# Kernel optimization log

Measured on AMD Instinct MI355X. Metric: run time of the kernel, lower is better.

Reference implementation:

```python
import jax, jax.numpy as jnp
import numpy as np

B, T, C = 1, 4096, 1024   # batch, seq, n_embd
E, K = 64, 8              # num_experts, router top-k
G, TG = 8, 4              # n_group, topk_group
H, HS = 512, 2048         # expert hidden, shared-expert hidden
STD = 0.02


def setup_inputs() -> dict:
    key = jax.random.key(0)
    ks = jax.random.split(key, 9)
    return {
        "x": jax.random.normal(ks[0], (B, T, C), jnp.float32),
        "router_w": jax.random.normal(ks[1], (E, C), jnp.float32) * (C ** -0.5),
        "e_bias": jnp.zeros((E,), jnp.float32),  # e_score_correction_bias buffer
        "gate_w": jax.random.normal(ks[2], (E, C, H), jnp.float32) * STD,
        "up_w": jax.random.normal(ks[3], (E, C, H), jnp.float32) * STD,
        "down_w": jax.random.normal(ks[4], (E, H, C), jnp.float32) * STD,
        "sh_gate_w": jax.random.normal(ks[5], (C, HS), jnp.float32) * STD,
        "sh_up_w": jax.random.normal(ks[6], (C, HS), jnp.float32) * STD,
        "sh_down_w": jax.random.normal(ks[7], (HS, C), jnp.float32) * STD,
    }


def _route(xf, router_w, e_bias):
    # grouped sigmoid top-k routing with score-correction bias (group_limited_greedy)
    S = xf.shape[0]
    scores = jax.nn.sigmoid(xf @ router_w.T)          # [S,E], raw sigmoid scores
    sb = scores + e_bias                               # biased scores (selection only)
    epg = E // G
    # per-group score = sum of top (K // topk_group) biased scores in that group
    grp = jax.lax.top_k(sb.reshape(S, G, epg), K // TG)[0].sum(-1)   # [S,G]
    gidx = jax.lax.top_k(grp, TG)[1]                                 # [S,TG]
    gmask = jnp.zeros((S, G), bool).at[jnp.arange(S)[:, None], gidx].set(True)
    emask = jnp.repeat(gmask, epg, axis=1)                           # [S,E]
    masked = jnp.where(emask, sb, -jnp.inf)
    topk_idx = jax.lax.top_k(masked, K)[1]                           # [S,K]
    w = jnp.take_along_axis(scores, topk_idx, axis=1)                # raw scores gathered
    w = w / (w.sum(-1, keepdims=True) + 1e-20)                       # norm_topk_prob
    return topk_idx, w


def reference(x, router_w, e_bias, gate_w, up_w, down_w, sh_gate_w, sh_up_w, sh_down_w):
    Bq, Tq, Cq = x.shape
    xf = x.reshape(Bq * Tq, Cq)
    # always-on shared expert (SwiGLU)
    shared = (jax.nn.silu(xf @ sh_gate_w) * (xf @ sh_up_w)) @ sh_down_w
    topk_idx, w = _route(xf, router_w, e_bias)
    fe = topk_idx.reshape(-1)                          # [S*K] expert id per routed row
    order = jnp.argsort(fe, stable=True)               # sort rows by expert (grouped)
    tok = order // K                                   # source token of each sorted row
    sorted_x = xf[tok]                                 # [S*K, C]
    group_sizes = jnp.bincount(fe, length=E).astype(jnp.int32)
    # grouped GEMMs (== torch._grouped_mm / bmm-over-buckets in the original)
    g = jax.lax.ragged_dot(sorted_x, gate_w, group_sizes)
    u = jax.lax.ragged_dot(sorted_x, up_w, group_sizes)
    h = jax.nn.silu(g) * u
    o = jax.lax.ragged_dot(h, down_w, group_sizes)     # [S*K, C]
    o = o * w.reshape(-1)[order][:, None]              # weight by routing prob
    routed = jnp.zeros_like(xf).at[tok].add(o)         # combine back per token
    return (shared + routed).reshape(Bq, Tq, Cq)
```

## Files before the change

kernel.cpp:

```cpp
#include <hip/hip_runtime.h>
#include <hip/hip_bf16.h>
#include <stdint.h>


#define S_TOK 4096
#define C_DIM 1024
#define E_NUM 64
#define H_DIM 512
#define HS_DIM 2048
#define ROWS_TOTAL (S_TOK * 8)
#define T_TILES 320
#define NB_ROUTED_F (T_TILES * 8)
#define NB_SHARED_F (32 * 32)
#define NB_ROUTED_D (T_TILES * 8)
#define NB_SHARED_D (32 * 8)
#define NB_SCATTER  (ROWS_TOTAL / 256)

typedef __attribute__((ext_vector_type(8))) short short8;
typedef __attribute__((ext_vector_type(4))) float f32x4;
typedef __attribute__((ext_vector_type(2))) unsigned int uint2v;

static __device__ __forceinline__ unsigned short f2bf(float f) {
    union { float f; uint32_t u; } v; v.f = f;
    uint32_t u = v.u;
    u += 0x7fffu + ((u >> 16) & 1u);
    return (unsigned short)(u >> 16);
}

static __device__ __forceinline__ uint32_t cvtpk(float a, float b) {
    uint32_t r;
    asm("v_cvt_pk_bf16_f32 %0, %1, %2" : "=v"(r) : "v"(a), "v"(b));
    return r;
}

static __device__ __forceinline__ void gl2lds16(const void* g, void* l) {
    __builtin_amdgcn_global_load_lds(
        (const __attribute__((address_space(1))) uint32_t*)g,
        (__attribute__((address_space(3))) uint32_t*)l, 16, 0, 0);
}

static __device__ __forceinline__ uint2v tr64(unsigned addr) {
    uint2v r;
    asm volatile("ds_read_b64_tr_b16 %0, %1" : "=v"(r) : "v"(addr));
    return r;
}

__global__ __launch_bounds__(256)
void router_topk_k(const float* __restrict__ x, const float* __restrict__ rw,
                   const float* __restrict__ ebias,
                   int* __restrict__ topk_idx, float* __restrict__ topk_w,
                   int* __restrict__ counts, int* __restrict__ done,
                   int* __restrict__ base, int* __restrict__ cursor,
                   int* __restrict__ tile_e, int* __restrict__ tile_m0) {
    int t0 = blockIdx.x * 32;
    __shared__ float xs[32][36];
    __shared__ float wsm[64][36];
    __shared__ float scf[32][64];
    __shared__ int last_blk;
    int t = threadIdx.x;
    int tx = t & 15, ty = t >> 4;
    float acc[2][4] = {};
    for (int k0 = 0; k0 < C_DIM; k0 += 32) {
        {
            int r = t >> 3, c = t & 7;
            *(float4*)&xs[r][c * 4] = *(const float4*)(x + (size_t)(t0 + r) * C_DIM + k0 + c * 4);
        }
        #pragma unroll
        for (int i = 0; i < 2; i++) {
            int idx = t + 256 * i;
            int r = idx >> 3, c = idx & 7;
            *(float4*)&wsm[r][c * 4] = *(const float4*)(rw + (size_t)r * C_DIM + k0 + c * 4);
        }
        __syncthreads();
        #pragma unroll
        for (int kk = 0; kk < 32; kk += 4) {
            float4 a0 = *(const float4*)&xs[ty * 2 + 0][kk];
            float4 a1 = *(const float4*)&xs[ty * 2 + 1][kk];
            #pragma unroll
            for (int j = 0; j < 4; j++) {
                float4 b = *(const float4*)&wsm[tx * 4 + j][kk];
                acc[0][j] += a0.x * b.x + a0.y * b.y + a0.z * b.z + a0.w * b.w;
                acc[1][j] += a1.x * b.x + a1.y * b.y + a1.z * b.z + a1.w * b.w;
            }
        }
        __syncthreads();
    }
    #pragma unroll
    for (int i = 0; i < 2; i++)
        #pragma unroll
        for (int j = 0; j < 4; j++)
            scf[ty * 2 + i][tx * 4 + j] = 1.f / (1.f + __expf(-acc[i][j]));
    __syncthreads();

    int lane = t & 63, w = t >> 6;
    float eb = ebias[lane];
    for (int r = 0; r < 8; r++) {
        int lt = w * 8 + r;
        int tok = t0 + lt;
        float sc = scf[lt][lane];
        float sb = sc + eb;
        float m1 = sb, m2 = -1e30f;
        #pragma unroll
        for (int off = 1; off <= 4; off <<= 1) {
            float o1 = __shfl_xor(m1, off);
            float o2 = __shfl_xor(m2, off);
            float hi = fmaxf(m1, o1), lo = fminf(m1, o1);
            m2 = fmaxf(lo, fmaxf(m2, o2));
            m1 = hi;
        }
        float grp = m1 + m2;
        float grpv[8];
        #pragma unroll
        for (int g = 0; g < 8; g++) grpv[g] = __shfl(grp, g * 8);
        unsigned gsel = 0;
        #pragma unroll
        for (int k = 0; k < 4; k++) {
            float best = -1e30f; int bi = 0;
            #pragma unroll
            for (int g = 0; g < 8; g++)
                if (!((gsel >> g) & 1) && grpv[g] > best) { best = grpv[g]; bi = g; }
            gsel |= 1u << bi;
        }
        float val = ((gsel >> (lane >> 3)) & 1) ? sb : -1e30f;
        int idx[8]; float sv[8]; float wsum = 0.f;
        #pragma unroll
        for (int k = 0; k < 8; k++) {
            uint32_t u = __float_as_uint(val);
            uint32_t mu = (u & 0x80000000u) ? ~u : (u | 0x80000000u);
            unsigned long long key = ((unsigned long long)mu << 6) | (unsigned long long)(63 - lane);
            #pragma unroll
            for (int off = 32; off; off >>= 1) {
                unsigned long long ok = __shfl_xor(key, off);
                if (ok > key) key = ok;
            }
            int win = 63 - (int)(key & 63ull);
            idx[k] = win;
            sv[k] = __shfl(sc, win);
            wsum += sv[k];
            if (lane == win) val = -1e30f;
        }
        float inv = 1.f / (wsum + 1e-20f);
        if (lane < 8) {
            topk_idx[tok * 8 + lane] = idx[lane];
            topk_w[tok * 8 + lane] = sv[lane] * inv;
            atomicAdd(&counts[idx[lane]], 1);
        }
    }

    __threadfence();
    __syncthreads();
    if (t == 0) last_blk = (atomicAdd(done, 1) == (int)gridDim.x - 1) ? 1 : 0;
    __syncthreads();
    if (last_blk && t < 64) {
        __threadfence();
        int e = t;
        int c = atomicAdd(&counts[e], 0);
        int s = c;
        #pragma unroll
        for (int off = 1; off < 64; off <<= 1) {
            int o = __shfl_up(s, off);
            if (e >= off) s += o;
        }
        int ex = s - c;
        base[e] = ex;
        cursor[e] = ex;
        int nt = (c + 127) >> 7;
        int ts = nt;
        #pragma unroll
        for (int off = 1; off < 64; off <<= 1) {
            int o = __shfl_up(ts, off);
            if (e >= off) ts += o;
        }
        int tb = ts - nt;
        for (int i = 0; i < nt; i++) { tile_e[tb + i] = e; tile_m0[tb + i] = i * 128; }
        int total = __shfl(ts, 63);
        for (int j = total + e; j < T_TILES; j += 64) tile_e[j] = -1;
    }
}

__global__ __launch_bounds__(256)
void scatter_cvt_k(const int* __restrict__ topk_idx, const float* __restrict__ topk_w,
                   int* __restrict__ cursor, int* __restrict__ row_token,
                   float* __restrict__ row_wgt, int* __restrict__ pos_of,
                   const float* __restrict__ i0, unsigned short* __restrict__ o0, int n0,
                   const float* __restrict__ i1, unsigned short* __restrict__ o1, int n1,
                   const float* __restrict__ i2, unsigned short* __restrict__ o2, int n2,
                   const float* __restrict__ i3, unsigned short* __restrict__ o3, int n3,
                   const float* __restrict__ i4, unsigned short* __restrict__ o4, int n4,
                   const float* __restrict__ i5, unsigned short* __restrict__ o5, int n5,
                   const float* __restrict__ i6, unsigned short* __restrict__ o6, int n6) {
    int bid = blockIdx.x;
    if (bid < NB_SCATTER) {
        int i = bid * 256 + threadIdx.x;
        int e = topk_idx[i];
        int pos = atomicAdd(&cursor[e], 1);
        row_token[pos] = i >> 3;
        row_wgt[pos] = topk_w[i];
        pos_of[i] = pos;
        return;
    }
    int g = (bid - NB_SCATTER) * 256 + threadIdx.x;
    const float* in; unsigned short* out;
    if (g < n0) { in = i0; out = o0; }
    else { g -= n0;
    if (g < n1) { in = i1; out = o1; }
    else { g -= n1;
    if (g < n2) { in = i2; out = o2; }
    else { g -= n2;
    if (g < n3) { in = i3; out = o3; }
    else { g -= n3;
    if (g < n4) { in = i4; out = o4; }
    else { g -= n4;
    if (g < n5) { in = i5; out = o5; }
    else { g -= n5;
    if (g >= n6) return;
    in = i6; out = o6; } } } } } }
    float4 v0 = ((const float4*)in)[4 * g];
    float4 v1 = ((const float4*)in)[4 * g + 1];
    float4 v2 = ((const float4*)in)[4 * g + 2];
    float4 v3 = ((const float4*)in)[4 * g + 3];
    uint32_t pk[8];
    pk[0] = cvtpk(v0.x, v0.y); pk[1] = cvtpk(v0.z, v0.w);
    pk[2] = cvtpk(v1.x, v1.y); pk[3] = cvtpk(v1.z, v1.w);
    pk[4] = cvtpk(v2.x, v2.y); pk[5] = cvtpk(v2.z, v2.w);
    pk[6] = cvtpk(v3.x, v3.y); pk[7] = cvtpk(v3.z, v3.w);
    ((uint4*)out)[2 * g]     = *(uint4*)&pk[0];
    ((uint4*)out)[2 * g + 1] = *(uint4*)&pk[4];
}

__global__ __launch_bounds__(256)
void combine_k(const float* __restrict__ O, const int* __restrict__ pos_of,
               float* __restrict__ out) {
    int t = blockIdx.x;
    int c = threadIdx.x;
    float4 s = ((const float4*)(out + (size_t)t * C_DIM))[c];
    int p[8];
    #pragma unroll
    for (int k = 0; k < 8; k++) p[k] = pos_of[t * 8 + k];
    #pragma unroll
    for (int k = 0; k < 8; k++) {
        float4 v = ((const float4*)(O + (size_t)p[k] * C_DIM))[c];
        s.x += v.x; s.y += v.y; s.z += v.z; s.w += v.w;
    }
    ((float4*)(out + (size_t)t * C_DIM))[c] = s;
}

__global__ __launch_bounds__(256, 3)
void fused_all_k(const short* __restrict__ xb,
                 const short* __restrict__ gate_b, const short* __restrict__ up_b,
                 const short* __restrict__ shg_b, const short* __restrict__ shu_b,
                 unsigned short* __restrict__ Hr, unsigned short* __restrict__ Hs,
                 const int* __restrict__ counts, const int* __restrict__ base,
                 const int* __restrict__ row_token,
                 const int* __restrict__ tile_e, const int* __restrict__ tile_m0) {
    constexpr int K = C_DIM;
    constexpr int NC = 4;

    int bid = blockIdx.x;
    bool routed = bid < NB_ROUTED_F;
    const short* B1; const short* B2; unsigned short* Cout;
    int m0, n0, Mrows, rowbase, N;
    if (routed) {
        int ti = bid >> 3;
        int e = tile_e[ti];
        if (e < 0) return;
        m0 = tile_m0[ti]; n0 = (bid & 7) * 64;
        Mrows = counts[e]; rowbase = base[e];
        N = H_DIM;
        B1 = gate_b + (size_t)e * H_DIM * K;
        B2 = up_b   + (size_t)e * H_DIM * K;
        Cout = Hr;
    } else {
        int s = bid - NB_ROUTED_F;
        m0 = (s >> 5) * 128; n0 = (s & 31) * 64;
        Mrows = S_TOK; rowbase = 0;
        N = HS_DIM;
        B1 = shg_b; B2 = shu_b;
        Cout = Hs;
    }

    __shared__ short As[3 * 4096];
    __shared__ short Bs1[3 * 2048];
    __shared__ short Bs2[3 * 2048];

    int tid = threadIdx.x;
    int lane = tid & 63, w = tid >> 6;
    int wr = w >> 1, wc = w & 1;
    int quad = lane >> 4, l16 = lane & 15;
    int sr = lane >> 2, sc = lane & 3;

    const short* aptr[2];
    #pragma unroll
    for (int i = 0; i < 2; i++) {
        int row = w * 32 + i * 16 + sr;
        int mrow = m0 + row;
        int cl = mrow < Mrows ? mrow : (Mrows - 1);
        size_t arow = routed ? (size_t)row_token[rowbase + cl] : (size_t)cl;
        aptr[i] = xb + arow * K + sc * 8;
    }

    const short* b1ptr;
    const short* b2ptr;
    {
        int L = lane;
        int r = (L & 7) >> 1, c = (L & 1) * 8;
        int kc = w * 2 + (L >> 5);
        int nc = (L >> 3) & 3;
        b1ptr = B1 + (size_t)(kc * 4 + r) * N + n0 + nc * 16 + c;
        b2ptr = B2 + (size_t)(kc * 4 + r) * N + n0 + nc * 16 + c;
    }
    const size_t bstep = (size_t)32 * N;

    f32x4 acc1[4][2] = {};
    f32x4 acc2[4][2] = {};

    const int nk = K >> 5;
    auto stage = [&](int slot) {
        #pragma unroll
        for (int i = 0; i < 2; i++) {
            gl2lds16(aptr[i], &As[slot * 4096 + (w * 32 + i * 16) * 32]);
            aptr[i] += 32;
        }
        gl2lds16(b1ptr, &Bs1[slot * 2048 + w * 512]); b1ptr += bstep;
        gl2lds16(b2ptr, &Bs2[slot * 2048 + w * 512]); b2ptr += bstep;
    };
    stage(0);
    stage(1);

    unsigned trb1 = (unsigned)(size_t)&Bs1[0] + (unsigned)(quad * 2 * NC * 128 + l16 * 8);
    unsigned trb2 = (unsigned)(size_t)&Bs2[0] + (unsigned)(quad * 2 * NC * 128 + l16 * 8);
    auto rdB = [&](unsigned trb, int slot, int nb) -> short8 {
        unsigned a0 = trb + (unsigned)(slot * 4096 + nb * 128);
        uint2v lo = tr64(a0);
        uint2v hi = tr64(a0 + NC * 128);
        union { uint32_t u[4]; short8 s; } u;
        u.u[0] = lo[0]; u.u[1] = lo[1]; u.u[2] = hi[0]; u.u[3] = hi[1];
        return u.s;
    };

    int slot = 0, nslot = 2;
    for (int t = 0; t < nk; t++) {
        if (t + 1 < nk) {
            asm volatile("s_waitcnt vmcnt(4)" ::: "memory");
        } else {
            asm volatile("s_waitcnt vmcnt(0)" ::: "memory");
        }
        __builtin_amdgcn_s_barrier();
        __builtin_amdgcn_sched_barrier(0);

        if (t + 2 < nk) stage(nslot);

        short8 a[4], b1[2], b2[2];
        #pragma unroll
        for (int i = 0; i < 4; i++)
            a[i] = *(const short8*)&As[slot * 4096 + (wr * 64 + i * 16 + l16) * 32 + quad * 8];
        #pragma unroll
        for (int j = 0; j < 2; j++) {
            int nb = wc * 2 + j;
            b1[j] = rdB(trb1, slot, nb);
            b2[j] = rdB(trb2, slot, nb);
        }
        asm volatile("s_waitcnt lgkmcnt(0)" ::: "memory");
        __builtin_amdgcn_sched_barrier(0);
        #pragma unroll
        for (int i = 0; i < 4; i++)
            #pragma unroll
            for (int j = 0; j < 2; j++) {
                acc1[i][j] = __builtin_amdgcn_mfma_f32_16x16x32_bf16(a[i], b1[j], acc1[i][j], 0, 0, 0);
                acc2[i][j] = __builtin_amdgcn_mfma_f32_16x16x32_bf16(a[i], b2[j], acc2[i][j], 0, 0, 0);
            }
        slot = (slot == 2) ? 0 : slot + 1;
        nslot = (nslot == 2) ? 0 : nslot + 1;
    }

    #pragma unroll
    for (int i = 0; i < 4; i++) {
        #pragma unroll
        for (int rr = 0; rr < 4; rr++) {
            int row = m0 + wr * 64 + i * 16 + quad * 4 + rr;
            if (row >= Mrows) continue;
            size_t orow = (size_t)(rowbase + row);
            #pragma unroll
            for (int j = 0; j < 2; j++) {
                int n = n0 + wc * 32 + j * 16 + l16;
                float v = acc1[i][j][rr];
                float u = acc2[i][j][rr];
                float h = v / (1.f + __expf(-v)) * u;
                Cout[orow * N + n] = f2bf(h);
            }
        }
    }
}

__global__ __launch_bounds__(256, 3)
void down_all_k(const short* __restrict__ Hr, const short* __restrict__ Hs,
                const short* __restrict__ down_b, const short* __restrict__ shd_b,
                float* __restrict__ O, float* __restrict__ out,
                const int* __restrict__ counts, const int* __restrict__ base,
                const float* __restrict__ row_wgt,
                const int* __restrict__ tile_e, const int* __restrict__ tile_m0) {
    constexpr int N = C_DIM;
    constexpr int NC = 8;
    constexpr int BS = 128 * 32;

    int bid = blockIdx.x;
    bool shared_e = bid < NB_SHARED_D;
    const short* A; const short* B1; float* Cout;
    int m0, n0, Mrows, rowbase, K;
    if (shared_e) {
        m0 = (bid >> 3) * 128; n0 = (bid & 7) * 128;
        Mrows = S_TOK; rowbase = 0;
        K = HS_DIM;
        A = Hs;
        B1 = shd_b;
        Cout = out;
    } else {
        int rb = bid - NB_SHARED_D;
        int ti = rb >> 3;
        int e = tile_e[ti];
        if (e < 0) return;
        m0 = tile_m0[ti]; n0 = (rb & 7) * 128;
        Mrows = counts[e]; rowbase = base[e];
        K = H_DIM;
        A = Hr;
        B1 = down_b + (size_t)e * N * H_DIM;
        Cout = O;
    }

    __shared__ short As[3 * 4096];
    __shared__ short Bs1[3 * BS];

    int tid = threadIdx.x;
    int lane = tid & 63, w = tid >> 6;
    int wr = w >> 1, wc = w & 1;
    int quad = lane >> 4, l16 = lane & 15;
    int sr = lane >> 2, sc = lane & 3;

    const short* aptr[2];
    #pragma unroll
    for (int i = 0; i < 2; i++) {
        int row = w * 32 + i * 16 + sr;
        int mrow = m0 + row;
        int cl = mrow < Mrows ? mrow : (Mrows - 1);
        aptr[i] = A + (size_t)(rowbase + cl) * K + sc * 8;
    }

    const short* b1ptr[2];
    {
        int L = lane;
        int r = (L & 7) >> 1, c = (L & 1) * 8;
        int nc = L >> 3;
        #pragma unroll
        for (int i = 0; i < 2; i++) {
            int kc = w * 2 + i;
            b1ptr[i] = B1 + (size_t)(kc * 4 + r) * N + n0 + nc * 16 + c;
        }
    }
    const size_t bstep = (size_t)32 * N;

    f32x4 acc1[4][4] = {};

    const int nk = K >> 5;
    auto stage = [&](int slot) {
        #pragma unroll
        for (int i = 0; i < 2; i++) {
            gl2lds16(aptr[i], &As[slot * 4096 + (w * 32 + i * 16) * 32]);
            aptr[i] += 32;
        }
        #pragma unroll
        for (int i = 0; i < 2; i++) {
            gl2lds16(b1ptr[i], &Bs1[slot * BS + (w * 2 + i) * 512]);
            b1ptr[i] += bstep;
        }
    };
    stage(0);
    stage(1);

    unsigned trb1 = (unsigned)(size_t)&Bs1[0] + (unsigned)(quad * 2 * NC * 128 + l16 * 8);
    auto rdB = [&](int slot, int nb) -> short8 {
        unsigned a0 = trb1 + (unsigned)(slot * BS * 2 + nb * 128);
        uint2v lo = tr64(a0);
        uint2v hi = tr64(a0 + NC * 128);
        union { uint32_t u[4]; short8 s; } u;
        u.u[0] = lo[0]; u.u[1] = lo[1]; u.u[2] = hi[0]; u.u[3] = hi[1];
        return u.s;
    };

    int slot = 0, nslot = 2;
    for (int t = 0; t < nk; t++) {
        if (t + 1 < nk) {
            asm volatile("s_waitcnt vmcnt(4)" ::: "memory");
        } else {
            asm volatile("s_waitcnt vmcnt(0)" ::: "memory");
        }
        __builtin_amdgcn_s_barrier();
        __builtin_amdgcn_sched_barrier(0);

        if (t + 2 < nk) stage(nslot);

        short8 a[4], b1[4];
        #pragma unroll
        for (int i = 0; i < 4; i++)
            a[i] = *(const short8*)&As[slot * 4096 + (wr * 64 + i * 16 + l16) * 32 + quad * 8];
        #pragma unroll
        for (int j = 0; j < 4; j++)
            b1[j] = rdB(slot, wc * 4 + j);
        asm volatile("s_waitcnt lgkmcnt(0)" ::: "memory");
        __builtin_amdgcn_sched_barrier(0);
        #pragma unroll
        for (int i = 0; i < 4; i++)
            #pragma unroll
            for (int j = 0; j < 4; j++)
                acc1[i][j] = __builtin_amdgcn_mfma_f32_16x16x32_bf16(a[i], b1[j], acc1[i][j], 0, 0, 0);
        slot = (slot == 2) ? 0 : slot + 1;
        nslot = (nslot == 2) ? 0 : nslot + 1;
    }

    #pragma unroll
    for (int i = 0; i < 4; i++) {
        #pragma unroll
        for (int rr = 0; rr < 4; rr++) {
            int row = m0 + wr * 64 + i * 16 + quad * 4 + rr;
            if (row >= Mrows) continue;
            size_t orow = (size_t)(rowbase + row);
            float scl = shared_e ? 1.f : row_wgt[rowbase + row];
            #pragma unroll
            for (int j = 0; j < 4; j++) {
                int n = n0 + wc * 64 + j * 16 + l16;
                Cout[orow * N + n] = acc1[i][j][rr] * scl;
            }
        }
    }
}

extern "C" void kernel_launch(void* const* d_in, const int* in_sizes, int n_in,
                              void* d_out, int out_size, void* d_ws, size_t ws_size,
                              hipStream_t stream) {
    const float* x        = (const float*)d_in[0];
    const float* router_w = (const float*)d_in[1];
    const float* e_bias   = (const float*)d_in[2];
    const float* gate_w   = (const float*)d_in[3];
    const float* up_w     = (const float*)d_in[4];
    const float* down_w   = (const float*)d_in[5];
    const float* sh_gate  = (const float*)d_in[6];
    const float* sh_up    = (const float*)d_in[7];
    const float* sh_down  = (const float*)d_in[8];
    float* out = (float*)d_out;
    char* ws = (char*)d_ws;

    int*   counts    = (int*)(ws);
    int*   base      = (int*)(ws + 256);
    int*   cursor    = (int*)(ws + 512);
    int*   done      = (int*)(ws + 768);
    int*   topk_idx  = (int*)(ws + 1024);
    float* topk_w    = (float*)(ws + 1024 + 131072);
    int*   row_token = (int*)(ws + 1024 + 2 * 131072);
    float* row_wgt   = (float*)(ws + 1024 + 3 * 131072);
    int*   pos_of    = (int*)(ws + 1664 * 1024);
    int*   tile_e    = (int*)(ws + 1800 * 1024);
    int*   tile_m0   = (int*)(ws + 1808 * 1024);
    const size_t MB = 1u << 20;
    unsigned short* xb        = (unsigned short*)(ws + 2 * MB);
    unsigned short* Hs        = (unsigned short*)(ws + 10 * MB);
    unsigned short* Hr        = (unsigned short*)(ws + 26 * MB);
    unsigned short* sh_gate_b = (unsigned short*)(ws + 58 * MB);
    unsigned short* sh_up_b   = (unsigned short*)(ws + 62 * MB);
    unsigned short* sh_down_b = (unsigned short*)(ws + 66 * MB);
    unsigned short* gate_b    = (unsigned short*)(ws + 70 * MB);
    unsigned short* up_b      = (unsigned short*)(ws + 134 * MB);
    unsigned short* down_b    = (unsigned short*)(ws + 198 * MB);
    float* O = (float*)(ws + 70 * MB);

    hipMemsetAsync(ws, 0, 1024, stream);

    router_topk_k<<<S_TOK / 32, 256, 0, stream>>>(
        x, router_w, e_bias, topk_idx, topk_w, counts, done,
        base, cursor, tile_e, tile_m0);

    const int NX = S_TOK * C_DIM / 16;
    const int NW = E_NUM * C_DIM * H_DIM / 16;
    const int NS = C_DIM * HS_DIM / 16;
    const int NTOT = NX + 3 * NW + 3 * NS;
    scatter_cvt_k<<<NB_SCATTER + (NTOT + 255) / 256, 256, 0, stream>>>(
        topk_idx, topk_w, cursor, row_token, row_wgt, pos_of,
        x, xb, NX, gate_w, gate_b, NW, up_w, up_b, NW, down_w, down_b, NW,
        sh_gate, sh_gate_b, NS, sh_up, sh_up_b, NS, sh_down, sh_down_b, NS);

    fused_all_k<<<NB_ROUTED_F + NB_SHARED_F, 256, 0, stream>>>(
        (const short*)xb, (const short*)gate_b, (const short*)up_b,
        (const short*)sh_gate_b, (const short*)sh_up_b, Hr, Hs,
        counts, base, row_token, tile_e, tile_m0);

    down_all_k<<<NB_SHARED_D + NB_ROUTED_D, 256, 0, stream>>>(
        (const short*)Hr, (const short*)Hs, (const short*)down_b, (const short*)sh_down_b,
        O, out, counts, base, row_wgt, tile_e, tile_m0);

    combine_k<<<S_TOK, 256, 0, stream>>>(O, pos_of, out);
}
```

Baseline: 888.3 us.

## Convert fp32 weights to bf16 inside GEMM kernels instead of a separate pass

Removes the separate conversion of all expert and shared weights to bf16 and has the gate/up and down GEMM kernels load fp32 weights directly into registers, convert them, and write swizzled bf16 tiles to LDS. The B path becomes register-staged double buffering in place of global_load_lds plus transposed LDS reads. This removes a full read-and-write pass over roughly 200MB of weights, but the GEMMs now read fp32 weights (twice the bytes), and weights shared by several tiles are read again as fp32. It also adds VALU conversion work and register pressure in the inner loop.

```diff
diff --git a/kernel.cpp b/kernel.cpp
--- a/kernel.cpp
+++ b/kernel.cpp
@@ -37,12 +37,6 @@
     __builtin_amdgcn_global_load_lds(
         (const __attribute__((address_space(1))) uint32_t*)g,
         (__attribute__((address_space(3))) uint32_t*)l, 16, 0, 0);
-}
-
-static __device__ __forceinline__ uint2v tr64(unsigned addr) {
-    uint2v r;
-    asm volatile("ds_read_b64_tr_b16 %0, %1" : "=v"(r) : "v"(addr));
-    return r;
 }
 
 __global__ __launch_bounds__(256)
@@ -179,16 +173,10 @@
 }
 
 __global__ __launch_bounds__(256)
-void scatter_cvt_k(const int* __restrict__ topk_idx, const float* __restrict__ topk_w,
-                   int* __restrict__ cursor, int* __restrict__ row_token,
-                   float* __restrict__ row_wgt, int* __restrict__ pos_of,
-                   const float* __restrict__ i0, unsigned short* __restrict__ o0, int n0,
-                   const float* __restrict__ i1, unsigned short* __restrict__ o1, int n1,
-                   const float* __restrict__ i2, unsigned short* __restrict__ o2, int n2,
-                   const float* __restrict__ i3, unsigned short* __restrict__ o3, int n3,
-                   const float* __restrict__ i4, unsigned short* __restrict__ o4, int n4,
-                   const float* __restrict__ i5, unsigned short* __restrict__ o5, int n5,
-                   const float* __restrict__ i6, unsigned short* __restrict__ o6, int n6) {
+void scatter_xcvt_k(const int* __restrict__ topk_idx, const float* __restrict__ topk_w,
+                    int* __restrict__ cursor, int* __restrict__ row_token,
+                    float* __restrict__ row_wgt, int* __restrict__ pos_of,
+                    const float* __restrict__ x, unsigned short* __restrict__ xb) {
     int bid = blockIdx.x;
     if (bid < NB_SCATTER) {
         int i = bid * 256 + threadIdx.x;
@@ -200,32 +188,17 @@
         return;
     }
     int g = (bid - NB_SCATTER) * 256 + threadIdx.x;
-    const float* in; unsigned short* out;
-    if (g < n0) { in = i0; out = o0; }
-    else { g -= n0;
-    if (g < n1) { in = i1; out = o1; }
-    else { g -= n1;
-    if (g < n2) { in = i2; out = o2; }
-    else { g -= n2;
-    if (g < n3) { in = i3; out = o3; }
-    else { g -= n3;
-    if (g < n4) { in = i4; out = o4; }
-    else { g -= n4;
-    if (g < n5) { in = i5; out = o5; }
-    else { g -= n5;
-    if (g >= n6) return;
-    in = i6; out = o6; } } } } } }
-    float4 v0 = ((const float4*)in)[4 * g];
-    float4 v1 = ((const float4*)in)[4 * g + 1];
-    float4 v2 = ((const float4*)in)[4 * g + 2];
-    float4 v3 = ((const float4*)in)[4 * g + 3];
+    float4 v0 = ((const float4*)x)[4 * g];
+    float4 v1 = ((const float4*)x)[4 * g + 1];
+    float4 v2 = ((const float4*)x)[4 * g + 2];
+    float4 v3 = ((const float4*)x)[4 * g + 3];
     uint32_t pk[8];
     pk[0] = cvtpk(v0.x, v0.y); pk[1] = cvtpk(v0.z, v0.w);
     pk[2] = cvtpk(v1.x, v1.y); pk[3] = cvtpk(v1.z, v1.w);
     pk[4] = cvtpk(v2.x, v2.y); pk[5] = cvtpk(v2.z, v2.w);
     pk[6] = cvtpk(v3.x, v3.y); pk[7] = cvtpk(v3.z, v3.w);
-    ((uint4*)out)[2 * g]     = *(uint4*)&pk[0];
-    ((uint4*)out)[2 * g + 1] = *(uint4*)&pk[4];
+    ((uint4*)xb)[2 * g]     = *(uint4*)&pk[0];
+    ((uint4*)xb)[2 * g + 1] = *(uint4*)&pk[4];
 }
 
 __global__ __launch_bounds__(256)
@@ -247,18 +220,17 @@
 
 __global__ __launch_bounds__(256, 3)
 void fused_all_k(const short* __restrict__ xb,
-                 const short* __restrict__ gate_b, const short* __restrict__ up_b,
-                 const short* __restrict__ shg_b, const short* __restrict__ shu_b,
+                 const float* __restrict__ gate_w, const float* __restrict__ up_w,
+                 const float* __restrict__ shg_w, const float* __restrict__ shu_w,
                  unsigned short* __restrict__ Hr, unsigned short* __restrict__ Hs,
                  const int* __restrict__ counts, const int* __restrict__ base,
                  const int* __restrict__ row_token,
                  const int* __restrict__ tile_e, const int* __restrict__ tile_m0) {
     constexpr int K = C_DIM;
-    constexpr int NC = 4;
 
     int bid = blockIdx.x;
     bool routed = bid < NB_ROUTED_F;
-    const short* B1; const short* B2; unsigned short* Cout;
+    const float* B1; const float* B2; unsigned short* Cout;
     int m0, n0, Mrows, rowbase, N;
     if (routed) {
         int ti = bid >> 3;
@@ -267,21 +239,21 @@
         m0 = tile_m0[ti]; n0 = (bid & 7) * 64;
         Mrows = counts[e]; rowbase = base[e];
         N = H_DIM;
-        B1 = gate_b + (size_t)e * H_DIM * K;
-        B2 = up_b   + (size_t)e * H_DIM * K;
+        B1 = gate_w + (size_t)e * K * H_DIM;
+        B2 = up_w   + (size_t)e * K * H_DIM;
         Cout = Hr;
     } else {
         int s = bid - NB_ROUTED_F;
         m0 = (s >> 5) * 128; n0 = (s & 31) * 64;
         Mrows = S_TOK; rowbase = 0;
         N = HS_DIM;
-        B1 = shg_b; B2 = shu_b;
+        B1 = shg_w; B2 = shu_w;
         Cout = Hs;
     }
 
     __shared__ short As[3 * 4096];
-    __shared__ short Bs1[3 * 2048];
-    __shared__ short Bs2[3 * 2048];
+    __shared__ short Bs1[2 * 2048];
+    __shared__ short Bs2[2 * 2048];
 
     int tid = threadIdx.x;
     int lane = tid & 63, w = tid >> 6;
@@ -299,56 +271,61 @@
         aptr[i] = xb + arow * K + sc * 8;
     }
 
-    const short* b1ptr;
-    const short* b2ptr;
-    {
-        int L = lane;
-        int r = (L & 7) >> 1, c = (L & 1) * 8;
-        int kc = w * 2 + (L >> 5);
-        int nc = (L >> 3) & 3;
-        b1ptr = B1 + (size_t)(kc * 4 + r) * N + n0 + nc * 16 + c;
-        b2ptr = B2 + (size_t)(kc * 4 + r) * N + n0 + nc * 16 + c;
-    }
-    const size_t bstep = (size_t)32 * N;
+    int nb = tid & 63, kg = tid >> 6;
+    const float* b1g = B1 + (size_t)(kg * 8) * N + n0 + nb;
+    const float* b2g = B2 + (size_t)(kg * 8) * N + n0 + nb;
+    const int bwr = nb * 32 + ((kg * 8) ^ ((nb & 3) << 3));
 
     f32x4 acc1[4][2] = {};
     f32x4 acc2[4][2] = {};
 
     const int nk = K >> 5;
-    auto stage = [&](int slot) {
+    auto stageA = [&](int slot) {
         #pragma unroll
         for (int i = 0; i < 2; i++) {
             gl2lds16(aptr[i], &As[slot * 4096 + (w * 32 + i * 16) * 32]);
             aptr[i] += 32;
         }
-        gl2lds16(b1ptr, &Bs1[slot * 2048 + w * 512]); b1ptr += bstep;
-        gl2lds16(b2ptr, &Bs2[slot * 2048 + w * 512]); b2ptr += bstep;
-    };
-    stage(0);
-    stage(1);
-
-    unsigned trb1 = (unsigned)(size_t)&Bs1[0] + (unsigned)(quad * 2 * NC * 128 + l16 * 8);
-    unsigned trb2 = (unsigned)(size_t)&Bs2[0] + (unsigned)(quad * 2 * NC * 128 + l16 * 8);
-    auto rdB = [&](unsigned trb, int slot, int nb) -> short8 {
-        unsigned a0 = trb + (unsigned)(slot * 4096 + nb * 128);
-        uint2v lo = tr64(a0);
-        uint2v hi = tr64(a0 + NC * 128);
-        union { uint32_t u[4]; short8 s; } u;
-        u.u[0] = lo[0]; u.u[1] = lo[1]; u.u[2] = hi[0]; u.u[3] = hi[1];
-        return u.s;
-    };
-
-    int slot = 0, nslot = 2;
-    for (int t = 0; t < nk; t++) {
-        if (t + 1 < nk) {
-            asm volatile("s_waitcnt vmcnt(4)" ::: "memory");
-        } else {
-            asm volatile("s_waitcnt vmcnt(0)" ::: "memory");
-        }
-        __builtin_amdgcn_s_barrier();
-        __builtin_amdgcn_sched_barrier(0);
-
-        if (t + 2 < nk) stage(nslot);
+    };
+    auto loadB = [&](float (&fb)[2][8]) {
+        #pragma unroll
+        for (int jj = 0; jj < 8; jj++) fb[0][jj] = b1g[(size_t)jj * N];
+        #pragma unroll
+        for (int jj = 0; jj < 8; jj++) fb[1][jj] = b2g[(size_t)jj * N];
+        b1g += (size_t)32 * N;
+        b2g += (size_t)32 * N;
+    };
+    auto writeB = [&](int buf, float (&fb)[2][8]) {
+        uint32_t w0[4], w1[4];
+        #pragma unroll
+        for (int q = 0; q < 4; q++) {
+            w0[q] = cvtpk(fb[0][2 * q], fb[0][2 * q + 1]);
+            w1[q] = cvtpk(fb[1][2 * q], fb[1][2 * q + 1]);
+        }
+        *(uint4*)&Bs1[buf * 2048 + bwr] = *(uint4*)w0;
+        *(uint4*)&Bs2[buf * 2048 + bwr] = *(uint4*)w1;
+    };
+
+    float fbA[2][8], fbB[2][8];
+    stageA(0);
+    stageA(1);
+    __builtin_amdgcn_sched_barrier(0);
+    {
+        float fb0[2][8];
+        loadB(fb0);
+        writeB(0, fb0);
+    }
+    __builtin_amdgcn_sched_barrier(0);
+    loadB(fbA);
+    asm volatile("s_waitcnt vmcnt(16) lgkmcnt(0)" ::: "memory");
+    __builtin_amdgcn_s_barrier();
+    __builtin_amdgcn_sched_barrier(0);
+
+    auto kstep = [&](int t, float (&fbIn)[2][8], float (&fbOut)[2][8]) {
+        int slot = t % 3;
+        int bbuf = t & 1;
+        bool pf = (t + 2 < nk);
+        if (pf) { stageA((t + 2) % 3); loadB(fbOut); }
 
         short8 a[4], b1[2], b2[2];
         #pragma unroll
@@ -356,12 +333,11 @@
             a[i] = *(const short8*)&As[slot * 4096 + (wr * 64 + i * 16 + l16) * 32 + quad * 8];
         #pragma unroll
         for (int j = 0; j < 2; j++) {
-            int nb = wc * 2 + j;
-            b1[j] = rdB(trb1, slot, nb);
-            b2[j] = rdB(trb2, slot, nb);
-        }
-        asm volatile("s_waitcnt lgkmcnt(0)" ::: "memory");
-        __builtin_amdgcn_sched_barrier(0);
+            int row = wc * 32 + j * 16 + l16;
+            int ro = row * 32 + ((quad * 8) ^ ((row & 3) << 3));
+            b1[j] = *(const short8*)&Bs1[bbuf * 2048 + ro];
+            b2[j] = *(const short8*)&Bs2[bbuf * 2048 + ro];
+        }
         #pragma unroll
         for (int i = 0; i < 4; i++)
             #pragma unroll
@@ -369,8 +345,18 @@
                 acc1[i][j] = __builtin_amdgcn_mfma_f32_16x16x32_bf16(a[i], b1[j], acc1[i][j], 0, 0, 0);
                 acc2[i][j] = __builtin_amdgcn_mfma_f32_16x16x32_bf16(a[i], b2[j], acc2[i][j], 0, 0, 0);
             }
-        slot = (slot == 2) ? 0 : slot + 1;
-        nslot = (nslot == 2) ? 0 : nslot + 1;
+        if (t + 1 < nk) {
+            writeB((t + 1) & 1, fbIn);
+            if (pf) asm volatile("s_waitcnt vmcnt(18) lgkmcnt(0)" ::: "memory");
+            else    asm volatile("s_waitcnt vmcnt(0) lgkmcnt(0)" ::: "memory");
+            __builtin_amdgcn_s_barrier();
+            __builtin_amdgcn_sched_barrier(0);
+        }
+    };
+
+    for (int t = 0; t < nk; t += 2) {
+        kstep(t, fbA, fbB);
+        if (t + 1 < nk) kstep(t + 1, fbB, fbA);
     }
 
     #pragma unroll
@@ -394,25 +380,23 @@
 
 __global__ __launch_bounds__(256, 3)
 void down_all_k(const short* __restrict__ Hr, const short* __restrict__ Hs,
-                const short* __restrict__ down_b, const short* __restrict__ shd_b,
+                const float* __restrict__ down_w, const float* __restrict__ shd_w,
                 float* __restrict__ O, float* __restrict__ out,
                 const int* __restrict__ counts, const int* __restrict__ base,
                 const float* __restrict__ row_wgt,
                 const int* __restrict__ tile_e, const int* __restrict__ tile_m0) {
     constexpr int N = C_DIM;
-    constexpr int NC = 8;
-    constexpr int BS = 128 * 32;
 
     int bid = blockIdx.x;
     bool shared_e = bid < NB_SHARED_D;
-    const short* A; const short* B1; float* Cout;
+    const short* A; const float* B1; float* Cout;
     int m0, n0, Mrows, rowbase, K;
     if (shared_e) {
         m0 = (bid >> 3) * 128; n0 = (bid & 7) * 128;
         Mrows = S_TOK; rowbase = 0;
         K = HS_DIM;
         A = Hs;
-        B1 = shd_b;
+        B1 = shd_w;
         Cout = out;
     } else {
         int rb = bid - NB_SHARED_D;
@@ -423,12 +407,12 @@
         Mrows = counts[e]; rowbase = base[e];
         K = H_DIM;
         A = Hr;
-        B1 = down_b + (size_t)e * N * H_DIM;
+        B1 = down_w + (size_t)e * H_DIM * N;
         Cout = O;
     }
 
     __shared__ short As[3 * 4096];
-    __shared__ short Bs1[3 * BS];
+    __shared__ short Bs1[2 * 4096];
 
     int tid = threadIdx.x;
     int lane = tid & 63, w = tid >> 6;
@@ -445,75 +429,86 @@
         aptr[i] = A + (size_t)(rowbase + cl) * K + sc * 8;
     }
 
-    const short* b1ptr[2];
-    {
-        int L = lane;
-        int r = (L & 7) >> 1, c = (L & 1) * 8;
-        int nc = L >> 3;
-        #pragma unroll
-        for (int i = 0; i < 2; i++) {
-            int kc = w * 2 + i;
-            b1ptr[i] = B1 + (size_t)(kc * 4 + r) * N + n0 + nc * 16 + c;
-        }
-    }
-    const size_t bstep = (size_t)32 * N;
+    int nb = tid & 63, kg = tid >> 6;
+    const float* b1g = B1 + (size_t)(kg * 8) * N + n0 + nb;
+    const int bwr = nb * 32 + ((kg * 8) ^ ((nb & 3) << 3));
 
     f32x4 acc1[4][4] = {};
 
     const int nk = K >> 5;
-    auto stage = [&](int slot) {
+    auto stageA = [&](int slot) {
         #pragma unroll
         for (int i = 0; i < 2; i++) {
             gl2lds16(aptr[i], &As[slot * 4096 + (w * 32 + i * 16) * 32]);
             aptr[i] += 32;
         }
-        #pragma unroll
-        for (int i = 0; i < 2; i++) {
-            gl2lds16(b1ptr[i], &Bs1[slot * BS + (w * 2 + i) * 512]);
-            b1ptr[i] += bstep;
-        }
-    };
-    stage(0);
-    stage(1);
-
-    unsigned trb1 = (unsigned)(size_t)&Bs1[0] + (unsigned)(quad * 2 * NC * 128 + l16 * 8);
-    auto rdB = [&](int slot, int nb) -> short8 {
-        unsigned a0 = trb1 + (unsigned)(slot * BS * 2 + nb * 128);
-        uint2v lo = tr64(a0);
-        uint2v hi = tr64(a0 + NC * 128);
-        union { uint32_t u[4]; short8 s; } u;
-        u.u[0] = lo[0]; u.u[1] = lo[1]; u.u[2] = hi[0]; u.u[3] = hi[1];
-        return u.s;
-    };
-
-    int slot = 0, nslot = 2;
-    for (int t = 0; t < nk; t++) {
-        if (t + 1 < nk) {
-            asm volatile("s_waitcnt vmcnt(4)" ::: "memory");
-        } else {
-            asm volatile("s_waitcnt vmcnt(0)" ::: "memory");
-        }
-        __builtin_amdgcn_s_barrier();
-        __builtin_amdgcn_sched_barrier(0);
-
-        if (t + 2 < nk) stage(nslot);
+    };
+    auto loadB = [&](float (&fb)[2][8]) {
+        #pragma unroll
+        for (int jj = 0; jj < 8; jj++) fb[0][jj] = b1g[(size_t)jj * N];
+        #pragma unroll
+        for (int jj = 0; jj < 8; jj++) fb[1][jj] = b1g[(size_t)jj * N + 64];
+        b1g += (size_t)32 * N;
+    };
+    auto writeB = [&](int buf, float (&fb)[2][8]) {
+        uint32_t w0[4], w1[4];
+        #pragma unroll
+        for (int q = 0; q < 4; q++) {
+            w0[q] = cvtpk(fb[0][2 * q], fb[0][2 * q + 1]);
+            w1[q] = cvtpk(fb[1][2 * q], fb[1][2 * q + 1]);
+        }
+        *(uint4*)&Bs1[buf * 4096 + bwr] = *(uint4*)w0;
+        *(uint4*)&Bs1[buf * 4096 + bwr + 64 * 32] = *(uint4*)w1;
+    };
+
+    float fbA[2][8], fbB[2][8];
+    stageA(0);
+    stageA(1);
+    __builtin_amdgcn_sched_barrier(0);
+    {
+        float fb0[2][8];
+        loadB(fb0);
+        writeB(0, fb0);
+    }
+    __builtin_amdgcn_sched_barrier(0);
+    loadB(fbA);
+    asm volatile("s_waitcnt vmcnt(16) lgkmcnt(0)" ::: "memory");
+    __builtin_amdgcn_s_barrier();
+    __builtin_amdgcn_sched_barrier(0);
+
+    auto kstep = [&](int t, float (&fbIn)[2][8], float (&fbOut)[2][8]) {
+        int slot = t % 3;
+        int bbuf = t & 1;
+        bool pf = (t + 2 < nk);
+        if (pf) { stageA((t + 2) % 3); loadB(fbOut); }
 
         short8 a[4], b1[4];
         #pragma unroll
         for (int i = 0; i < 4; i++)
             a[i] = *(const short8*)&As[slot * 4096 + (wr * 64 + i * 16 + l16) * 32 + quad * 8];
         #pragma unroll
-        for (int j = 0; j < 4; j++)
-            b1[j] = rdB(slot, wc * 4 + j);
-        asm volatile("s_waitcnt lgkmcnt(0)" ::: "memory");
-        __builtin_amdgcn_sched_barrier(0);
+        for (int j = 0; j < 4; j++) {
+            int row = wc * 64 + j * 16 + l16;
+            int ro = row * 32 + ((quad * 8) ^ ((row & 3) << 3));
+            b1[j] = *(const short8*)&Bs1[bbuf * 4096 + ro];
+        }
         #pragma unroll
         for (int i = 0; i < 4; i++)
             #pragma unroll
             for (int j = 0; j < 4; j++)
                 acc1[i][j] = __builtin_amdgcn_mfma_f32_16x16x32_bf16(a[i], b1[j], acc1[i][j], 0, 0, 0);
-        slot = (slot == 2) ? 0 : slot + 1;
-        nslot = (nslot == 2) ? 0 : nslot + 1;
+        if (t + 1 < nk) {
+            writeB((t + 1) & 1, fbIn);
+            if (pf) asm volatile("s_waitcnt vmcnt(18) lgkmcnt(0)" ::: "memory");
+            else    asm volatile("s_waitcnt vmcnt(0) lgkmcnt(0)" ::: "memory");
+            __builtin_amdgcn_s_barrier();
+            __builtin_amdgcn_sched_barrier(0);
+        }
+    };
+
+    for (int t = 0; t < nk; t += 2) {
+        kstep(t, fbA, fbB);
+        if (t + 1 < nk) kstep(t + 1, fbB, fbA);
     }
 
     #pragma unroll
@@ -560,16 +555,10 @@
     int*   tile_e    = (int*)(ws + 1800 * 1024);
     int*   tile_m0   = (int*)(ws + 1808 * 1024);
     const size_t MB = 1u << 20;
-    unsigned short* xb        = (unsigned short*)(ws + 2 * MB);
-    unsigned short* Hs        = (unsigned short*)(ws + 10 * MB);
-    unsigned short* Hr        = (unsigned short*)(ws + 26 * MB);
-    unsigned short* sh_gate_b = (unsigned short*)(ws + 58 * MB);
-    unsigned short* sh_up_b   = (unsigned short*)(ws + 62 * MB);
-    unsigned short* sh_down_b = (unsigned short*)(ws + 66 * MB);
-    unsigned short* gate_b    = (unsigned short*)(ws + 70 * MB);
-    unsigned short* up_b      = (unsigned short*)(ws + 134 * MB);
-    unsigned short* down_b    = (unsigned short*)(ws + 198 * MB);
-    float* O = (float*)(ws + 70 * MB);
+    unsigned short* xb = (unsigned short*)(ws + 2 * MB);
+    unsigned short* Hs = (unsigned short*)(ws + 10 * MB);
+    unsigned short* Hr = (unsigned short*)(ws + 26 * MB);
+    float*          O  = (float*)(ws + 70 * MB);
 
     hipMemsetAsync(ws, 0, 1024, stream);
 
@@ -578,21 +567,15 @@
         base, cursor, tile_e, tile_m0);
 
     const int NX = S_TOK * C_DIM / 16;
-    const int NW = E_NUM * C_DIM * H_DIM / 16;
-    const int NS = C_DIM * HS_DIM / 16;
-    const int NTOT = NX + 3 * NW + 3 * NS;
-    scatter_cvt_k<<<NB_SCATTER + (NTOT + 255) / 256, 256, 0, stream>>>(
-        topk_idx, topk_w, cursor, row_token, row_wgt, pos_of,
-        x, xb, NX, gate_w, gate_b, NW, up_w, up_b, NW, down_w, down_b, NW,
-        sh_gate, sh_gate_b, NS, sh_up, sh_up_b, NS, sh_down, sh_down_b, NS);
+    scatter_xcvt_k<<<NB_SCATTER + NX / 256, 256, 0, stream>>>(
+        topk_idx, topk_w, cursor, row_token, row_wgt, pos_of, x, xb);
 
     fused_all_k<<<NB_ROUTED_F + NB_SHARED_F, 256, 0, stream>>>(
-        (const short*)xb, (const short*)gate_b, (const short*)up_b,
-        (const short*)sh_gate_b, (const short*)sh_up_b, Hr, Hs,
+        (const short*)xb, gate_w, up_w, sh_gate, sh_up, Hr, Hs,
         counts, base, row_token, tile_e, tile_m0);
 
     down_all_k<<<NB_SHARED_D + NB_ROUTED_D, 256, 0, stream>>>(
-        (const short*)Hr, (const short*)Hs, (const short*)down_b, (const short*)sh_down_b,
+        (const short*)Hr, (const short*)Hs, down_w, sh_down,
         O, out, counts, base, row_wgt, tile_e, tile_m0);
 
     combine_k<<<S_TOK, 256, 0, stream>>>(O, pos_of, out);
```

After: 829.0 us. 6.7% less time.
